# Kernel optimization log

Measured on AMD Instinct MI355X. Metric: run time of the kernel, lower is better.

The kernel has to match this reference:

```python
import jax, jax.numpy as jnp
import numpy as np

FEAT = 7  # hard-coded last-dim split in the original module


def setup_inputs() -> dict:
    key = jax.random.key(0)
    k1, k2, k3 = jax.random.split(key, 3)
    B, L, D = 16, 2048, 448  # D must be divisible by 7
    return {
        "queries": jax.random.normal(k1, (B, L, D), dtype=jnp.float32),
        "keys": jax.random.normal(k2, (B, L, D), dtype=jnp.float32),
        "values": jax.random.normal(k3, (B, L, D), dtype=jnp.float32),
        "attn_mask": jnp.zeros((1,), dtype=bool),  # unused (mask_flag=False)
    }


def reference(queries, keys, values, attn_mask):
    B, L, D = queries.shape
    E = D // FEAT
    # view(B, L, E, 7)
    q = queries.reshape(B, L, E, FEAT)
    k = keys.reshape(B, L, E, FEAT)
    v = values.reshape(B, L, E, FEAT)

    # scores_time = einsum('bler,bsep->bls'): r and p are independently summed,
    # so this factorizes as (sum_r q) @ (sum_p k)^T over e.
    q_t = q.sum(axis=-1)            # [B, L, E]
    k_t = k.sum(axis=-1)            # [B, S, E]
    scores_time = jnp.einsum('ble,bse->bls', q_t, k_t)   # [B, L, S]
    A_time = jax.nn.softmax(scores_time, axis=-2)        # softmax over L (dim=-2)

    # scores_feature = einsum('bler,bsep->brp'): l and s summed independently.
    q_f = q.sum(axis=1)             # [B, E, R]
    k_f = k.sum(axis=1)             # [B, E, P]
    scores_feature = jnp.einsum('ber,bep->brp', q_f, k_f)  # [B, 7, 7]
    A_feature = jax.nn.softmax(scores_feature, axis=-2)    # softmax over r (dim=-2)

    # A_time_feature = einsum('bls,brp->blr'): s and p summed independently.
    A_tf = A_time.sum(axis=-1)[:, :, None] * A_feature.sum(axis=-1)[:, None, :]  # [B, L, 7]
    A_tf = jax.nn.softmax(A_tf.reshape(B, L * FEAT), axis=-1).reshape(B, L, FEAT)

    # V = einsum('bsep,blr->bler'): s and p summed from values -> outer product.
    v_sum = v.sum(axis=(1, 3))      # [B, E]
    V = A_tf[:, :, None, :] * v_sum[:, None, :, None]  # [B, L, E, 7]
    return V.reshape(B, L, D)
```

## Files before the change

kernel.cpp:

```cpp
#include <hip/hip_runtime.h>
#include <math.h>

#define LL 2048
#define EE 64
#define FF 7
#define DD 448

#define OFF_QT 0
#define OFF_KT 2097152
#define OFF_QF 4194304
#define OFF_KF 4201472
#define OFF_VS 4208640
#define OFF_AF 4209664
#define OFF_CM 4209776
#define OFF_CZ 4242544
#define OFF_AT 4275312
#define OFF_MS 4308080
#define OFF_CMP 4308112
#define OFF_CZP 4570256

__global__ __launch_bounds__(256) void k_reduce_qk(const float* __restrict__ src,
                                                   float* __restrict__ t_out,
                                                   float* __restrict__ f_out) {
    __shared__ float buf[16 * DD];
    int blk = blockIdx.x;
    int b = blk >> 7;
    int l0 = (blk & 127) << 4;
    const float4* s4 = (const float4*)(src + ((size_t)b * LL + l0) * DD);
    float4* b4 = (float4*)buf;
#pragma unroll
    for (int i = 0; i < 7; i++) b4[threadIdx.x + 256 * i] = s4[threadIdx.x + 256 * i];
    __syncthreads();
    int e = threadIdx.x & 63, g = threadIdx.x >> 6;
    float fa[7] = {0.f, 0.f, 0.f, 0.f, 0.f, 0.f, 0.f};
    for (int rr = g; rr < 16; rr += 4) {
        float s = 0.f;
#pragma unroll
        for (int r = 0; r < 7; r++) { float v = buf[rr * DD + e * 7 + r]; s += v; fa[r] += v; }
        t_out[((size_t)b * LL + l0 + rr) * EE + e] = s;
    }
    __syncthreads();
#pragma unroll
    for (int r = 0; r < 7; r++) buf[(g * 64 + e) * 7 + r] = fa[r];
    __syncthreads();
    if (g == 0) {
#pragma unroll
        for (int r = 0; r < 7; r++) {
            float s = buf[e * 7 + r] + buf[(64 + e) * 7 + r] + buf[(128 + e) * 7 + r] + buf[(192 + e) * 7 + r];
            atomicAdd(&f_out[(b * EE + e) * 7 + r], s);
        }
    }
}

__global__ __launch_bounds__(256) void k_reduce_v(const float* __restrict__ src,
                                                  float* __restrict__ vs) {
    __shared__ float buf[16 * DD];
    int blk = blockIdx.x;
    int b = blk >> 7;
    int l0 = (blk & 127) << 4;
    const float4* s4 = (const float4*)(src + ((size_t)b * LL + l0) * DD);
    float4* b4 = (float4*)buf;
#pragma unroll
    for (int i = 0; i < 7; i++) b4[threadIdx.x + 256 * i] = s4[threadIdx.x + 256 * i];
    __syncthreads();
    int e = threadIdx.x & 63, g = threadIdx.x >> 6;
    float a = 0.f;
    for (int rr = g; rr < 16; rr += 4) {
#pragma unroll
        for (int r = 0; r < 7; r++) a += buf[rr * DD + e * 7 + r];
    }
    __syncthreads();
    buf[g * 64 + e] = a;
    __syncthreads();
    if (g == 0) atomicAdd(&vs[b * EE + e], buf[e] + buf[64 + e] + buf[128 + e] + buf[192 + e]);
}

__global__ void k_feat(const float* __restrict__ qf, const float* __restrict__ kf,
                       float* __restrict__ af) {
    __shared__ float qs[448], ks[448], sf[49], A[49];
    int b = blockIdx.x, t = threadIdx.x;
    for (int i = t; i < 448; i += 64) { qs[i] = qf[b * 448 + i]; ks[i] = kf[b * 448 + i]; }
    __syncthreads();
    if (t < 49) {
        int r = t / 7, p = t % 7;
        float s = 0.f;
        for (int e = 0; e < 64; e++) s += qs[e * 7 + r] * ks[e * 7 + p];
        sf[t] = s;
    }
    __syncthreads();
    if (t < 7) {
        float m = -1e30f;
        for (int r = 0; r < 7; r++) m = fmaxf(m, sf[r * 7 + t]);
        float z = 0.f;
        for (int r = 0; r < 7; r++) z += __expf(sf[r * 7 + t] - m);
        float iz = 1.f / z;
        for (int r = 0; r < 7; r++) A[r * 7 + t] = __expf(sf[r * 7 + t] - m) * iz;
    }
    __syncthreads();
    if (t < 7) {
        float s = 0.f;
        for (int p = 0; p < 7; p++) s += A[t * 7 + p];
        af[b * 7 + t] = s;
    }
}

__global__ __launch_bounds__(256) void k_colstats(const float* __restrict__ qt,
                                                  const float* __restrict__ kt,
                                                  float* __restrict__ cmp,
                                                  float* __restrict__ czp) {
    __shared__ __align__(16) float kb[128 * 68];
    __shared__ __align__(16) float qb[64 * 68];
    int bid = blockIdx.x;
    int b = bid >> 7, cc = (bid >> 3) & 15, lc = bid & 7;
    int c0 = cc << 7, lbase = lc << 8;
    int tid = threadIdx.x, tc = tid & 15, tr = tid >> 4;
    for (int idx = tid; idx < 2048; idx += 256) {
        int c = idx >> 4, e4 = (idx & 15) << 2;
        *(float4*)(kb + c * 68 + e4) =
            *(const float4*)(kt + ((size_t)(b * LL + c0 + c)) * EE + e4);
    }
    float m[8], s[8];
#pragma unroll
    for (int j = 0; j < 8; j++) { m[j] = -1e30f; s[j] = 0.f; }
    for (int lt = 0; lt < 4; lt++) {
        __syncthreads();
        for (int idx = tid; idx < 1024; idx += 256) {
            int r = idx >> 4, e4 = (idx & 15) << 2;
            *(float4*)(qb + r * 68 + e4) =
                *(const float4*)(qt + ((size_t)(b * LL + lbase + lt * 64 + r)) * EE + e4);
        }
        __syncthreads();
        float acc[4][8];
#pragma unroll
        for (int i = 0; i < 4; i++)
#pragma unroll
            for (int j = 0; j < 8; j++) acc[i][j] = 0.f;
#pragma unroll
        for (int e = 0; e < 64; e += 4) {
            float4 qv[4], kv[8];
#pragma unroll
            for (int i = 0; i < 4; i++) qv[i] = *(const float4*)(qb + (i * 16 + tr) * 68 + e);
#pragma unroll
            for (int j = 0; j < 8; j++) kv[j] = *(const float4*)(kb + (j * 16 + tc) * 68 + e);
#pragma unroll
            for (int i = 0; i < 4; i++)
#pragma unroll
                for (int j = 0; j < 8; j++) {
                    acc[i][j] += qv[i].x * kv[j].x;
                    acc[i][j] += qv[i].y * kv[j].y;
                    acc[i][j] += qv[i].z * kv[j].z;
                    acc[i][j] += qv[i].w * kv[j].w;
                }
        }
#pragma unroll
        for (int j = 0; j < 8; j++) {
            float tm = fmaxf(fmaxf(acc[0][j], acc[1][j]), fmaxf(acc[2][j], acc[3][j]));
            if (tm > m[j]) { s[j] *= __expf(m[j] - tm); m[j] = tm; }
#pragma unroll
            for (int i = 0; i < 4; i++) s[j] += __expf(acc[i][j] - m[j]);
        }
    }
    __syncthreads();
    float* mred = kb;
    float* sred = kb + 2048;
#pragma unroll
    for (int j = 0; j < 8; j++) {
        mred[tr * 128 + j * 16 + tc] = m[j];
        sred[tr * 128 + j * 16 + tc] = s[j];
    }
    __syncthreads();
    if (tid < 128) {
        float M = -1e30f, Z = 0.f;
        for (int g = 0; g < 16; g++) {
            float mg = mred[g * 128 + tid], sg = sred[g * 128 + tid];
            float nm = fmaxf(M, mg);
            Z = Z * __expf(M - nm) + sg * __expf(mg - nm);
            M = nm;
        }
        cmp[((size_t)(b * 8 + lc)) * LL + c0 + tid] = M;
        czp[((size_t)(b * 8 + lc)) * LL + c0 + tid] = Z;
    }
}

__global__ __launch_bounds__(256) void k_colmerge(const float* __restrict__ cmp,
                                                  const float* __restrict__ czp,
                                                  float* __restrict__ cm,
                                                  float* __restrict__ cz) {
    int idx = blockIdx.x * 256 + threadIdx.x;
    int b = idx >> 11, s = idx & 2047;
    float mp[8], zp[8];
#pragma unroll
    for (int lc = 0; lc < 8; lc++) {
        mp[lc] = cmp[((size_t)(b * 8 + lc)) * LL + s];
        zp[lc] = czp[((size_t)(b * 8 + lc)) * LL + s];
    }
    float M = mp[0];
#pragma unroll
    for (int lc = 1; lc < 8; lc++) M = fmaxf(M, mp[lc]);
    float Z = 0.f;
#pragma unroll
    for (int lc = 0; lc < 8; lc++) Z += zp[lc] * __expf(mp[lc] - M);
    cm[idx] = M;
    cz[idx] = 1.f / Z;
}

__global__ __launch_bounds__(256) void k_rowsum(const float* __restrict__ qt,
                                                const float* __restrict__ kt,
                                                const float* __restrict__ cm,
                                                const float* __restrict__ cz,
                                                float* __restrict__ at) {
    __shared__ __align__(16) float qb[128 * 68];
    __shared__ __align__(16) float kb[64 * 68];
    __shared__ float mt[64], zt[64];
    int bid = blockIdx.x;
    int b = bid >> 7, rc = (bid >> 3) & 15, sc = bid & 7;
    int l0 = rc << 7, sbase = sc << 8;
    int tid = threadIdx.x, tl = tid & 15, tg = tid >> 4;
    for (int idx = tid; idx < 2048; idx += 256) {
        int r = idx >> 4, e4 = (idx & 15) << 2;
        *(float4*)(qb + r * 68 + e4) =
            *(const float4*)(qt + ((size_t)(b * LL + l0 + r)) * EE + e4);
    }
    float rs[8] = {0.f, 0.f, 0.f, 0.f, 0.f, 0.f, 0.f, 0.f};
    for (int st = 0; st < 4; st++) {
        __syncthreads();
        for (int idx = tid; idx < 1024; idx += 256) {
            int c = idx >> 4, e4 = (idx & 15) << 2;
            *(float4*)(kb + c * 68 + e4) =
                *(const float4*)(kt + ((size_t)(b * LL + sbase + st * 64 + c)) * EE + e4);
        }
        if (tid < 64) {
            mt[tid] = cm[b * LL + sbase + st * 64 + tid];
            zt[tid] = cz[b * LL + sbase + st * 64 + tid];
        }
        __syncthreads();
        float acc[8][4];
#pragma unroll
        for (int j = 0; j < 8; j++)
#pragma unroll
            for (int i = 0; i < 4; i++) acc[j][i] = 0.f;
#pragma unroll
        for (int e = 0; e < 64; e += 4) {
            float4 qv[8], kv[4];
#pragma unroll
            for (int j = 0; j < 8; j++) qv[j] = *(const float4*)(qb + (j * 16 + tl) * 68 + e);
#pragma unroll
            for (int i = 0; i < 4; i++) kv[i] = *(const float4*)(kb + (i * 16 + tg) * 68 + e);
#pragma unroll
            for (int j = 0; j < 8; j++)
#pragma unroll
                for (int i = 0; i < 4; i++) {
                    acc[j][i] += qv[j].x * kv[i].x;
                    acc[j][i] += qv[j].y * kv[i].y;
                    acc[j][i] += qv[j].z * kv[i].z;
                    acc[j][i] += qv[j].w * kv[i].w;
                }
        }
#pragma unroll
        for (int j = 0; j < 8; j++)
#pragma unroll
            for (int i = 0; i < 4; i++) {
                int c = i * 16 + tg;
                rs[j] += __expf(acc[j][i] - mt[c]) * zt[c];
            }
    }
    __syncthreads();
    float* red = qb;
#pragma unroll
    for (int j = 0; j < 8; j++) red[tg * 128 + j * 16 + tl] = rs[j];
    __syncthreads();
    if (tid < 128) {
        float ssum = 0.f;
        for (int g = 0; g < 16; g++) ssum += red[g * 128 + tid];
        atomicAdd(at + (size_t)b * LL + l0 + tid, ssum);
    }
}

__global__ __launch_bounds__(256) void k_batchstats(const float* __restrict__ at,
                                                    const float* __restrict__ af,
                                                    float* __restrict__ ms) {
    __shared__ float red[256];
    __shared__ float afs[7];
    int b = blockIdx.x, t = threadIdx.x;
    if (t < 7) afs[t] = af[b * 7 + t];
    float mx = -1e30f;
    for (int l = t; l < LL; l += 256) mx = fmaxf(mx, at[(size_t)b * LL + l]);
    red[t] = mx;
    __syncthreads();
    for (int o = 128; o > 0; o >>= 1) {
        if (t < o) red[t] = fmaxf(red[t], red[t + o]);
        __syncthreads();
    }
    float mxat = red[0];
    __syncthreads();
    float mxaf = afs[0];
#pragma unroll
    for (int r = 1; r < 7; r++) mxaf = fmaxf(mxaf, afs[r]);
    float M = mxat * mxaf;
    float s = 0.f;
    for (int l = t; l < LL; l += 256) {
        float a = at[(size_t)b * LL + l];
#pragma unroll
        for (int r = 0; r < 7; r++) s += __expf(a * afs[r] - M);
    }
    red[t] = s;
    __syncthreads();
    for (int o = 128; o > 0; o >>= 1) {
        if (t < o) red[t] += red[t + o];
        __syncthreads();
    }
    if (t == 0) { ms[b * 2] = M; ms[b * 2 + 1] = 1.f / red[0]; }
}

__global__ __launch_bounds__(256) void k_out(const float* __restrict__ at,
                                             const float* __restrict__ af,
                                             const float* __restrict__ vs,
                                             const float* __restrict__ ms,
                                             float* __restrict__ out) {
    __shared__ __align__(16) float sm[4 * DD];
    int row0 = blockIdx.x << 2;
    int tid = threadIdx.x;
    int g = tid >> 6, e = tid & 63;
    int row = row0 + g;
    int b = row >> 11;
    float a = at[row];
    float M = ms[b * 2], iS = ms[b * 2 + 1];
    float v = vs[b * EE + e] * iS;
#pragma unroll
    for (int r = 0; r < 7; r++) sm[g * DD + e * 7 + r] = __expf(a * af[b * 7 + r] - M) * v;
    __syncthreads();
    float4* o4 = (float4*)(out + (size_t)row0 * DD);
    const float4* s4 = (const float4*)sm;
    for (int i = tid; i < 448; i += 256) o4[i] = s4[i];
}

extern "C" void kernel_launch(void* const* d_in, const int* in_sizes, int n_in,
                              void* d_out, int out_size, void* d_ws, size_t ws_size,
                              hipStream_t stream) {
    const float* q = (const float*)d_in[0];
    const float* k = (const float*)d_in[1];
    const float* v = (const float*)d_in[2];
    float* out = (float*)d_out;
    float* ws = (float*)d_ws;

    float* qt = ws + OFF_QT;
    float* kt = ws + OFF_KT;
    float* qf = ws + OFF_QF;
    float* kf = ws + OFF_KF;
    float* vs = ws + OFF_VS;
    float* af = ws + OFF_AF;
    float* cm = ws + OFF_CM;
    float* cz = ws + OFF_CZ;
    float* at = ws + OFF_AT;
    float* ms = ws + OFF_MS;
    float* cmp = ws + OFF_CMP;
    float* czp = ws + OFF_CZP;

    hipMemsetAsync(qf, 0, (7168 + 7168 + 1024) * sizeof(float), stream);
    hipMemsetAsync(at, 0, 32768 * sizeof(float), stream);

    k_reduce_qk<<<2048, 256, 0, stream>>>(q, qt, qf);
    k_reduce_qk<<<2048, 256, 0, stream>>>(k, kt, kf);
    k_reduce_v<<<2048, 256, 0, stream>>>(v, vs);
    k_feat<<<16, 64, 0, stream>>>(qf, kf, af);
    k_colstats<<<2048, 256, 0, stream>>>(qt, kt, cmp, czp);
    k_colmerge<<<128, 256, 0, stream>>>(cmp, czp, cm, cz);
    k_rowsum<<<2048, 256, 0, stream>>>(qt, kt, cm, cz, at);
    k_batchstats<<<16, 256, 0, stream>>>(at, af, ms);
    k_out<<<8192, 256, 0, stream>>>(at, af, vs, ms, out);
}
```

Baseline: 545.6 us.

## Fuse reduction kernels and retile score kernels to 128x128 single-pass tiles

Measured after the change: 498.2 us. 1.1x faster.

```diff
diff --git a/kernel.cpp b/kernel.cpp
--- a/kernel.cpp
+++ b/kernel.cpp
@@ -16,14 +16,20 @@
 #define OFF_CZ 4242544
 #define OFF_AT 4275312
 #define OFF_MS 4308080
-#define OFF_CMP 4308112
-#define OFF_CZP 4570256
-
-__global__ __launch_bounds__(256) void k_reduce_qk(const float* __restrict__ src,
-                                                   float* __restrict__ t_out,
-                                                   float* __restrict__ f_out) {
+
+__global__ __launch_bounds__(256) void k_prep(const float* __restrict__ q,
+                                              const float* __restrict__ k,
+                                              const float* __restrict__ v,
+                                              float* __restrict__ qt,
+                                              float* __restrict__ kt,
+                                              float* __restrict__ qf,
+                                              float* __restrict__ kf,
+                                              float* __restrict__ vs) {
     __shared__ float buf[16 * DD];
     int blk = blockIdx.x;
+    int which = blk >> 11;
+    blk &= 2047;
+    const float* src = which == 0 ? q : (which == 1 ? k : v);
     int b = blk >> 7;
     int l0 = (blk & 127) << 4;
     const float4* s4 = (const float4*)(src + ((size_t)b * LL + l0) * DD);
@@ -32,47 +38,38 @@
     for (int i = 0; i < 7; i++) b4[threadIdx.x + 256 * i] = s4[threadIdx.x + 256 * i];
     __syncthreads();
     int e = threadIdx.x & 63, g = threadIdx.x >> 6;
-    float fa[7] = {0.f, 0.f, 0.f, 0.f, 0.f, 0.f, 0.f};
-    for (int rr = g; rr < 16; rr += 4) {
-        float s = 0.f;
-#pragma unroll
-        for (int r = 0; r < 7; r++) { float v = buf[rr * DD + e * 7 + r]; s += v; fa[r] += v; }
-        t_out[((size_t)b * LL + l0 + rr) * EE + e] = s;
-    }
-    __syncthreads();
-#pragma unroll
-    for (int r = 0; r < 7; r++) buf[(g * 64 + e) * 7 + r] = fa[r];
-    __syncthreads();
-    if (g == 0) {
-#pragma unroll
-        for (int r = 0; r < 7; r++) {
-            float s = buf[e * 7 + r] + buf[(64 + e) * 7 + r] + buf[(128 + e) * 7 + r] + buf[(192 + e) * 7 + r];
-            atomicAdd(&f_out[(b * EE + e) * 7 + r], s);
+    if (which < 2) {
+        float* t_out = which ? kt : qt;
+        float* f_out = which ? kf : qf;
+        float fa[7] = {0.f, 0.f, 0.f, 0.f, 0.f, 0.f, 0.f};
+        for (int rr = g; rr < 16; rr += 4) {
+            float s = 0.f;
+#pragma unroll
+            for (int r = 0; r < 7; r++) { float x = buf[rr * DD + e * 7 + r]; s += x; fa[r] += x; }
+            t_out[((size_t)b * LL + l0 + rr) * EE + e] = s;
         }
-    }
-}
-
-__global__ __launch_bounds__(256) void k_reduce_v(const float* __restrict__ src,
-                                                  float* __restrict__ vs) {
-    __shared__ float buf[16 * DD];
-    int blk = blockIdx.x;
-    int b = blk >> 7;
-    int l0 = (blk & 127) << 4;
-    const float4* s4 = (const float4*)(src + ((size_t)b * LL + l0) * DD);
-    float4* b4 = (float4*)buf;
-#pragma unroll
-    for (int i = 0; i < 7; i++) b4[threadIdx.x + 256 * i] = s4[threadIdx.x + 256 * i];
-    __syncthreads();
-    int e = threadIdx.x & 63, g = threadIdx.x >> 6;
-    float a = 0.f;
-    for (int rr = g; rr < 16; rr += 4) {
-#pragma unroll
-        for (int r = 0; r < 7; r++) a += buf[rr * DD + e * 7 + r];
-    }
-    __syncthreads();
-    buf[g * 64 + e] = a;
-    __syncthreads();
-    if (g == 0) atomicAdd(&vs[b * EE + e], buf[e] + buf[64 + e] + buf[128 + e] + buf[192 + e]);
+        __syncthreads();
+#pragma unroll
+        for (int r = 0; r < 7; r++) buf[(g * 64 + e) * 7 + r] = fa[r];
+        __syncthreads();
+        if (g == 0) {
+#pragma unroll
+            for (int r = 0; r < 7; r++) {
+                float s = buf[e * 7 + r] + buf[(64 + e) * 7 + r] + buf[(128 + e) * 7 + r] + buf[(192 + e) * 7 + r];
+                atomicAdd(&f_out[(b * EE + e) * 7 + r], s);
+            }
+        }
+    } else {
+        float a = 0.f;
+        for (int rr = g; rr < 16; rr += 4) {
+#pragma unroll
+            for (int r = 0; r < 7; r++) a += buf[rr * DD + e * 7 + r];
+        }
+        __syncthreads();
+        buf[g * 64 + e] = a;
+        __syncthreads();
+        if (g == 0) atomicAdd(&vs[b * EE + e], buf[e] + buf[64 + e] + buf[128 + e] + buf[192 + e]);
+    }
 }
 
 __global__ void k_feat(const float* __restrict__ qf, const float* __restrict__ kf,
@@ -104,81 +101,74 @@
     }
 }
 
-__global__ __launch_bounds__(256) void k_colstats(const float* __restrict__ qt,
-                                                  const float* __restrict__ kt,
-                                                  float* __restrict__ cmp,
-                                                  float* __restrict__ czp) {
+__global__ __launch_bounds__(256, 2) void k_colstats(const float* __restrict__ qt,
+                                                     const float* __restrict__ kt,
+                                                     float* __restrict__ cmp,
+                                                     float* __restrict__ czp) {
     __shared__ __align__(16) float kb[128 * 68];
-    __shared__ __align__(16) float qb[64 * 68];
+    __shared__ __align__(16) float qb[128 * 68];
     int bid = blockIdx.x;
-    int b = bid >> 7, cc = (bid >> 3) & 15, lc = bid & 7;
-    int c0 = cc << 7, lbase = lc << 8;
+    int b = bid >> 8, cc = (bid >> 4) & 15, rc = bid & 15;
+    int c0 = cc << 7, l0 = rc << 7;
     int tid = threadIdx.x, tc = tid & 15, tr = tid >> 4;
     for (int idx = tid; idx < 2048; idx += 256) {
-        int c = idx >> 4, e4 = (idx & 15) << 2;
-        *(float4*)(kb + c * 68 + e4) =
-            *(const float4*)(kt + ((size_t)(b * LL + c0 + c)) * EE + e4);
+        int r = idx >> 4, e4 = (idx & 15) << 2;
+        *(float4*)(kb + r * 68 + e4) = *(const float4*)(kt + ((size_t)(b * LL + c0 + r)) * EE + e4);
+        *(float4*)(qb + r * 68 + e4) = *(const float4*)(qt + ((size_t)(b * LL + l0 + r)) * EE + e4);
+    }
+    __syncthreads();
+    float acc[8][8];
+#pragma unroll
+    for (int i = 0; i < 8; i++)
+#pragma unroll
+        for (int j = 0; j < 8; j++) acc[i][j] = 0.f;
+#pragma unroll
+    for (int e = 0; e < 64; e += 4) {
+        float4 qv[8], kv[8];
+#pragma unroll
+        for (int i = 0; i < 8; i++) qv[i] = *(const float4*)(qb + (i * 16 + tr) * 68 + e);
+#pragma unroll
+        for (int j = 0; j < 8; j++) kv[j] = *(const float4*)(kb + (j * 16 + tc) * 68 + e);
+#pragma unroll
+        for (int i = 0; i < 8; i++)
+#pragma unroll
+            for (int j = 0; j < 8; j++) {
+                acc[i][j] += qv[i].x * kv[j].x;
+                acc[i][j] += qv[i].y * kv[j].y;
+                acc[i][j] += qv[i].z * kv[j].z;
+                acc[i][j] += qv[i].w * kv[j].w;
+            }
     }
     float m[8], s[8];
 #pragma unroll
-    for (int j = 0; j < 8; j++) { m[j] = -1e30f; s[j] = 0.f; }
-    for (int lt = 0; lt < 4; lt++) {
-        __syncthreads();
-        for (int idx = tid; idx < 1024; idx += 256) {
-            int r = idx >> 4, e4 = (idx & 15) << 2;
-            *(float4*)(qb + r * 68 + e4) =
-                *(const float4*)(qt + ((size_t)(b * LL + lbase + lt * 64 + r)) * EE + e4);
-        }
-        __syncthreads();
-        float acc[4][8];
-#pragma unroll
-        for (int i = 0; i < 4; i++)
-#pragma unroll
-            for (int j = 0; j < 8; j++) acc[i][j] = 0.f;
-#pragma unroll
-        for (int e = 0; e < 64; e += 4) {
-            float4 qv[4], kv[8];
-#pragma unroll
-            for (int i = 0; i < 4; i++) qv[i] = *(const float4*)(qb + (i * 16 + tr) * 68 + e);
-#pragma unroll
-            for (int j = 0; j < 8; j++) kv[j] = *(const float4*)(kb + (j * 16 + tc) * 68 + e);
-#pragma unroll
-            for (int i = 0; i < 4; i++)
-#pragma unroll
-                for (int j = 0; j < 8; j++) {
-                    acc[i][j] += qv[i].x * kv[j].x;
-                    acc[i][j] += qv[i].y * kv[j].y;
-                    acc[i][j] += qv[i].z * kv[j].z;
-                    acc[i][j] += qv[i].w * kv[j].w;
-                }
-        }
-#pragma unroll
-        for (int j = 0; j < 8; j++) {
-            float tm = fmaxf(fmaxf(acc[0][j], acc[1][j]), fmaxf(acc[2][j], acc[3][j]));
-            if (tm > m[j]) { s[j] *= __expf(m[j] - tm); m[j] = tm; }
-#pragma unroll
-            for (int i = 0; i < 4; i++) s[j] += __expf(acc[i][j] - m[j]);
-        }
-    }
-    __syncthreads();
-    float* mred = kb;
-    float* sred = kb + 2048;
-#pragma unroll
     for (int j = 0; j < 8; j++) {
-        mred[tr * 128 + j * 16 + tc] = m[j];
-        sred[tr * 128 + j * 16 + tc] = s[j];
+        float m01 = fmaxf(acc[0][j], acc[1][j]), m23 = fmaxf(acc[2][j], acc[3][j]);
+        float m45 = fmaxf(acc[4][j], acc[5][j]), m67 = fmaxf(acc[6][j], acc[7][j]);
+        m[j] = fmaxf(fmaxf(m01, m23), fmaxf(m45, m67));
+        float z = 0.f;
+#pragma unroll
+        for (int i = 0; i < 8; i++) z += __expf(acc[i][j] - m[j]);
+        s[j] = z;
+    }
+    __syncthreads();
+    float* mred = qb;
+    float* sred = kb;
+#pragma unroll
+    for (int j = 0; j < 8; j++) {
+        mred[tr * 132 + j * 16 + tc] = m[j];
+        sred[tr * 132 + j * 16 + tc] = s[j];
     }
     __syncthreads();
     if (tid < 128) {
         float M = -1e30f, Z = 0.f;
         for (int g = 0; g < 16; g++) {
-            float mg = mred[g * 128 + tid], sg = sred[g * 128 + tid];
+            float mg = mred[g * 132 + tid], sg = sred[g * 132 + tid];
             float nm = fmaxf(M, mg);
             Z = Z * __expf(M - nm) + sg * __expf(mg - nm);
             M = nm;
         }
-        cmp[((size_t)(b * 8 + lc)) * LL + c0 + tid] = M;
-        czp[((size_t)(b * 8 + lc)) * LL + c0 + tid] = Z;
+        cmp[((size_t)(b * 16 + rc)) * LL + c0 + tid] = M;
+        czp[((size_t)(b * 16 + rc)) * LL + c0 + tid] = Z;
     }
 }
 
@@ -188,90 +178,79 @@
                                                   float* __restrict__ cz) {
     int idx = blockIdx.x * 256 + threadIdx.x;
     int b = idx >> 11, s = idx & 2047;
-    float mp[8], zp[8];
-#pragma unroll
-    for (int lc = 0; lc < 8; lc++) {
-        mp[lc] = cmp[((size_t)(b * 8 + lc)) * LL + s];
-        zp[lc] = czp[((size_t)(b * 8 + lc)) * LL + s];
-    }
-    float M = mp[0];
-#pragma unroll
-    for (int lc = 1; lc < 8; lc++) M = fmaxf(M, mp[lc]);
-    float Z = 0.f;
-#pragma unroll
-    for (int lc = 0; lc < 8; lc++) Z += zp[lc] * __expf(mp[lc] - M);
+    float M = -1e30f, Z = 0.f;
+#pragma unroll
+    for (int p = 0; p < 16; p++) {
+        float mg = cmp[((size_t)(b * 16 + p)) * LL + s];
+        float zg = czp[((size_t)(b * 16 + p)) * LL + s];
+        float nm = fmaxf(M, mg);
+        Z = Z * __expf(M - nm) + zg * __expf(mg - nm);
+        M = nm;
+    }
     cm[idx] = M;
     cz[idx] = 1.f / Z;
 }
 
-__global__ __launch_bounds__(256) void k_rowsum(const float* __restrict__ qt,
-                                                const float* __restrict__ kt,
-                                                const float* __restrict__ cm,
-                                                const float* __restrict__ cz,
-                                                float* __restrict__ at) {
+__global__ __launch_bounds__(256, 2) void k_rowsum(const float* __restrict__ qt,
+                                                   const float* __restrict__ kt,
+                                                   const float* __restrict__ cm,
+                                                   const float* __restrict__ cz,
+                                                   float* __restrict__ at) {
+    __shared__ __align__(16) float kb[128 * 68];
     __shared__ __align__(16) float qb[128 * 68];
-    __shared__ __align__(16) float kb[64 * 68];
-    __shared__ float mt[64], zt[64];
+    __shared__ float mt[128], zt[128];
     int bid = blockIdx.x;
-    int b = bid >> 7, rc = (bid >> 3) & 15, sc = bid & 7;
-    int l0 = rc << 7, sbase = sc << 8;
-    int tid = threadIdx.x, tl = tid & 15, tg = tid >> 4;
+    int b = bid >> 8, rc = (bid >> 4) & 15, sc = bid & 15;
+    int l0 = rc << 7, c0 = sc << 7;
+    int tid = threadIdx.x, tc = tid & 15, tr = tid >> 4;
     for (int idx = tid; idx < 2048; idx += 256) {
         int r = idx >> 4, e4 = (idx & 15) << 2;
-        *(float4*)(qb + r * 68 + e4) =
-            *(const float4*)(qt + ((size_t)(b * LL + l0 + r)) * EE + e4);
+        *(float4*)(kb + r * 68 + e4) = *(const float4*)(kt + ((size_t)(b * LL + c0 + r)) * EE + e4);
+        *(float4*)(qb + r * 68 + e4) = *(const float4*)(qt + ((size_t)(b * LL + l0 + r)) * EE + e4);
+    }
+    if (tid < 128) {
+        mt[tid] = cm[b * LL + c0 + tid];
+        zt[tid] = cz[b * LL + c0 + tid];
+    }
+    __syncthreads();
+    float acc[8][8];
+#pragma unroll
+    for (int i = 0; i < 8; i++)
+#pragma unroll
+        for (int j = 0; j < 8; j++) acc[i][j] = 0.f;
+#pragma unroll
+    for (int e = 0; e < 64; e += 4) {
+        float4 qv[8], kv[8];
+#pragma unroll
+        for (int i = 0; i < 8; i++) qv[i] = *(const float4*)(qb + (i * 16 + tr) * 68 + e);
+#pragma unroll
+        for (int j = 0; j < 8; j++) kv[j] = *(const float4*)(kb + (j * 16 + tc) * 68 + e);
+#pragma unroll
+        for (int i = 0; i < 8; i++)
+#pragma unroll
+            for (int j = 0; j < 8; j++) {
+                acc[i][j] += qv[i].x * kv[j].x;
+                acc[i][j] += qv[i].y * kv[j].y;
+                acc[i][j] += qv[i].z * kv[j].z;
+                acc[i][j] += qv[i].w * kv[j].w;
+            }
     }
     float rs[8] = {0.f, 0.f, 0.f, 0.f, 0.f, 0.f, 0.f, 0.f};
-    for (int st = 0; st < 4; st++) {
-        __syncthreads();
-        for (int idx = tid; idx < 1024; idx += 256) {
-            int c = idx >> 4, e4 = (idx & 15) << 2;
-            *(float4*)(kb + c * 68 + e4) =
-                *(const float4*)(kt + ((size_t)(b * LL + sbase + st * 64 + c)) * EE + e4);
-        }
-        if (tid < 64) {
-            mt[tid] = cm[b * LL + sbase + st * 64 + tid];
-            zt[tid] = cz[b * LL + sbase + st * 64 + tid];
-        }
-        __syncthreads();
-        float acc[8][4];
-#pragma unroll
-        for (int j = 0; j < 8; j++)
-#pragma unroll
-            for (int i = 0; i < 4; i++) acc[j][i] = 0.f;
-#pragma unroll
-        for (int e = 0; e < 64; e += 4) {
-            float4 qv[8], kv[4];
-#pragma unroll
-            for (int j = 0; j < 8; j++) qv[j] = *(const float4*)(qb + (j * 16 + tl) * 68 + e);
-#pragma unroll
-            for (int i = 0; i < 4; i++) kv[i] = *(const float4*)(kb + (i * 16 + tg) * 68 + e);
-#pragma unroll
-            for (int j = 0; j < 8; j++)
-#pragma unroll
-                for (int i = 0; i < 4; i++) {
-                    acc[j][i] += qv[j].x * kv[i].x;
-                    acc[j][i] += qv[j].y * kv[i].y;
-                    acc[j][i] += qv[j].z * kv[i].z;
-                    acc[j][i] += qv[j].w * kv[i].w;
-                }
-        }
-#pragma unroll
-        for (int j = 0; j < 8; j++)
-#pragma unroll
-            for (int i = 0; i < 4; i++) {
-                int c = i * 16 + tg;
-                rs[j] += __expf(acc[j][i] - mt[c]) * zt[c];
-            }
+#pragma unroll
+    for (int j = 0; j < 8; j++) {
+        int c = j * 16 + tc;
+        float mc = mt[c], zc = zt[c];
+#pragma unroll
+        for (int i = 0; i < 8; i++) rs[i] += __expf(acc[i][j] - mc) * zc;
     }
     __syncthreads();
     float* red = qb;
 #pragma unroll
-    for (int j = 0; j < 8; j++) red[tg * 128 + j * 16 + tl] = rs[j];
+    for (int i = 0; i < 8; i++) red[tc * 132 + i * 16 + tr] = rs[i];
     __syncthreads();
     if (tid < 128) {
         float ssum = 0.f;
-        for (int g = 0; g < 16; g++) ssum += red[g * 128 + tid];
+        for (int g = 0; g < 16; g++) ssum += red[g * 132 + tid];
         atomicAdd(at + (size_t)b * LL + l0 + tid, ssum);
     }
 }
@@ -353,19 +332,17 @@
     float* cz = ws + OFF_CZ;
     float* at = ws + OFF_AT;
     float* ms = ws + OFF_MS;
-    float* cmp = ws + OFF_CMP;
-    float* czp = ws + OFF_CZP;
+    float* cmp = out;
+    float* czp = out + 524288;
 
     hipMemsetAsync(qf, 0, (7168 + 7168 + 1024) * sizeof(float), stream);
     hipMemsetAsync(at, 0, 32768 * sizeof(float), stream);
 
-    k_reduce_qk<<<2048, 256, 0, stream>>>(q, qt, qf);
-    k_reduce_qk<<<2048, 256, 0, stream>>>(k, kt, kf);
-    k_reduce_v<<<2048, 256, 0, stream>>>(v, vs);
+    k_prep<<<6144, 256, 0, stream>>>(q, k, v, qt, kt, qf, kf, vs);
     k_feat<<<16, 64, 0, stream>>>(qf, kf, af);
-    k_colstats<<<2048, 256, 0, stream>>>(qt, kt, cmp, czp);
+    k_colstats<<<4096, 256, 0, stream>>>(qt, kt, cmp, czp);
     k_colmerge<<<128, 256, 0, stream>>>(cmp, czp, cm, cz);
-    k_rowsum<<<2048, 256, 0, stream>>>(qt, kt, cm, cz, at);
+    k_rowsum<<<4096, 256, 0, stream>>>(qt, kt, cm, cz, at);
     k_batchstats<<<16, 256, 0, stream>>>(at, af, ms);
     k_out<<<8192, 256, 0, stream>>>(at, af, vs, ms, out);
 }
```
